# Optimization experiments

Measured on AMD Instinct MI355X. Metric: run time of the kernel, lower is better.

## Reference

```python
import jax, jax.numpy as jnp
import numpy as np

LATENT_N = 1024
COMMITMENT_COST = 1.0
TEMP = 0.1


def setup_inputs() -> dict:
    key = jax.random.key(0)
    k0, k1, k2, k3, k4, k5 = jax.random.split(key, 6)
    N, D, H, Fd, K = 65536, 1024, 128, 512, LATENT_N
    input_data = jax.random.normal(k0, (N, D), dtype=jnp.float32)
    W1 = jax.random.normal(k1, (D, H), dtype=jnp.float32) * (1.0 / np.sqrt(D))
    b1 = jnp.zeros((H,), dtype=jnp.float32)
    W2 = jax.random.normal(k2, (H, Fd), dtype=jnp.float32) * (1.0 / np.sqrt(H))
    b2 = jnp.zeros((Fd,), dtype=jnp.float32)
    code_book = jax.random.uniform(k3, (K, Fd), dtype=jnp.float32,
                                   minval=-1.0 / K, maxval=1.0 / K)
    return {"input_data": input_data, "W1": W1, "b1": b1,
            "W2": W2, "b2": b2, "code_book": code_book}


def reference(input_data, W1, b1, W2, b2, code_book):
    # feat MLP: Linear -> ReLU -> Linear
    z = jnp.matmul(jnp.maximum(jnp.matmul(input_data, W1) + b1, 0.0), W2) + b2  # [N, F]
    # squared L2 distances to codebook entries: [N, K]
    distances = (jnp.sum(z * z, axis=1, keepdims=True)
                 + jnp.sum(code_book * code_book, axis=1)
                 - 2.0 * jnp.matmul(z, code_book.T))
    logits = -distances / TEMP
    # categorical sample per row (softmax of logits)
    idx = jax.random.categorical(jax.random.key(42), logits, axis=-1)  # [N] int
    encodings = jax.nn.one_hot(idx, LATENT_N, dtype=z.dtype)  # [N, K]
    quantized = jnp.matmul(encodings, code_book)  # [N, F] == code_book[idx]
    e_latent_loss = jnp.mean((jax.lax.stop_gradient(quantized) - z) ** 2)
    q_latent_loss = jnp.mean((quantized - jax.lax.stop_gradient(z)) ** 2)
    loss = q_latent_loss + COMMITMENT_COST * e_latent_loss
    # straight-through estimator
    quantized_st = z + jax.lax.stop_gradient(quantized - z)
    avg_probs = jnp.mean(encodings, axis=0)  # [K]
    perplexity = jnp.exp(-jnp.sum(avg_probs * jnp.log(avg_probs + 1e-10)))
    return (loss, quantized_st, perplexity, encodings, -distances)
```

## Files before the change

kernel.cpp:

```cpp
#include <hip/hip_runtime.h>
#include <stdint.h>

#define N_ROWS 65536
#define DIM 1024
#define HID 128
#define FD 512
#define KCB 1024
#define HALFCNT 33554432u

#define OFF_Q    1
#define OFF_PERP 33554433
#define OFF_ENC  33554434
#define OFF_ND   100663298

typedef __attribute__((ext_vector_type(8))) short sh8;
typedef __attribute__((ext_vector_type(4))) float f32x4;

__device__ __forceinline__ uint32_t rotl32(uint32_t v, int r) { return (v << r) | (v >> (32 - r)); }

__device__ __forceinline__ void threefry(uint32_t c0, uint32_t c1, uint32_t& o0, uint32_t& o1) {
    const uint32_t ks0 = 0u, ks1 = 42u, ks2 = 0x1BD11BDAu ^ 0u ^ 42u;
    uint32_t x0 = c0 + ks0, x1 = c1 + ks1;
#define TFR(r) x0 += x1; x1 = rotl32(x1, r); x1 ^= x0;
    TFR(13) TFR(15) TFR(26) TFR(6)  x0 += ks1; x1 += ks2 + 1u;
    TFR(17) TFR(29) TFR(16) TFR(24) x0 += ks2; x1 += ks0 + 2u;
    TFR(13) TFR(15) TFR(26) TFR(6)  x0 += ks0; x1 += ks1 + 3u;
    TFR(17) TFR(29) TFR(16) TFR(24) x0 += ks1; x1 += ks2 + 4u;
    TFR(13) TFR(15) TFR(26) TFR(6)  x0 += ks2; x1 += ks0 + 5u;
#undef TFR
    o0 = x0; o1 = x1;
}

__device__ __forceinline__ float gumbel_f32(uint32_t b) {
    uint32_t m = b >> 9;
    float u = m ? (float)m * 1.1920928955078125e-07f : 1.17549435e-38f;
    const float LN2 = 0.6931471805599453f;
    return -LN2 * __log2f(-LN2 * __log2f(u));
}

__device__ __forceinline__ ushort bf16rne(float f) {
    uint32_t u = __float_as_uint(f);
    return (ushort)((u + 0x7FFFu + ((u >> 16) & 1u)) >> 16);
}
__device__ __forceinline__ uint32_t pack2rne(float a, float b) {
    return (uint32_t)bf16rne(a) | ((uint32_t)bf16rne(b) << 16);
}

__device__ __forceinline__ void async_cp16(const void* g, void* l) {
    __builtin_amdgcn_global_load_lds(
        (const __attribute__((address_space(1))) void*)g,
        (__attribute__((address_space(3))) void*)l, 16, 0, 0);
}

__global__ __launch_bounds__(256) void k_prep(const float* __restrict__ cb, const float* __restrict__ W1,
                                              const float* __restrict__ W2,
                                              ushort* __restrict__ cbh, double* __restrict__ cc,
                                              ushort* __restrict__ w1th, ushort* __restrict__ w2th,
                                              int* __restrict__ counts, double* __restrict__ lossb) {
    int gb = blockIdx.x, t = threadIdx.x;
    if (gb < 256) {
        int k = gb * 4 + (t >> 6), l = t & 63;
        const float4* row = (const float4*)(cb + (size_t)k * FD);
        float4 a = row[l * 2], b = row[l * 2 + 1];
        float v[8] = {a.x, a.y, a.z, a.w, b.x, b.y, b.z, b.w};
        double s = 0.0;
        uint32_t hu[4];
        #pragma unroll
        for (int e = 0; e < 4; ++e) {
            hu[e] = pack2rne(v[2 * e], v[2 * e + 1]);
            s = fma((double)v[2 * e], (double)v[2 * e], s);
            s = fma((double)v[2 * e + 1], (double)v[2 * e + 1], s);
        }
        *(uint4*)(cbh + (size_t)k * FD + l * 8) = make_uint4(hu[0], hu[1], hu[2], hu[3]);
        for (int off = 32; off; off >>= 1) s += __shfl_down(s, off, 64);
        if (l == 0) cc[k] = s;
    } else if (gb < 384) {
        int c = gb - 256;
        #pragma unroll
        for (int u = 0; u < 4; ++u) {
            int k = t + u * 256;
            w1th[(size_t)c * DIM + k] = bf16rne(W1[(size_t)k * HID + c]);
        }
    } else if (gb < 640) {
        int c = (gb - 384) * 2 + (t >> 7);
        int tt = t & 127;
        w2th[(size_t)c * HID + tt] = bf16rne(W2[(size_t)tt * FD + c]);
    } else {
        for (int k = t; k < KCB; k += 256) counts[k] = 0;
        lossb[t] = 0.0;
    }
}

__global__ __launch_bounds__(256) void kA(const float* __restrict__ X, const ushort* __restrict__ w1th,
                                          const float* __restrict__ b1, ushort* __restrict__ hh) {
    __shared__ __align__(16) char lds[32768];
    int t = threadIdx.x;
    int lane = t & 63, w = t >> 6;
    int wr = w >> 1, wc = w & 1;
    int n0 = blockIdx.x * 128;
    f32x4 zero4 = {0.f, 0.f, 0.f, 0.f};
    f32x4 acc[4][4];
    #pragma unroll
    for (int i = 0; i < 4; ++i)
        #pragma unroll
        for (int j = 0; j < 4; ++j) acc[i][j] = zero4;

    int xr = t >> 1;
    int cb0 = (t & 1) * 4;
    int xsw = xr & 7;

    for (int k0 = 0; k0 < DIM; k0 += 64) {
        #pragma unroll
        for (int i = 0; i < 4; ++i) {
            int rr = w * 32 + i * 8;
            int row = rr + (lane >> 3);
            int csrc = (lane & 7) ^ (row & 7);
            size_t goff = (size_t)row * DIM + k0 + csrc * 8;
            async_cp16(w1th + goff, lds + 16384 + rr * 128);
        }
        const float* xp = X + (size_t)(n0 + xr) * DIM + k0 + cb0 * 8;
        #pragma unroll
        for (int c = 0; c < 4; ++c) {
            float4 a = *(const float4*)(xp + c * 8);
            float4 b = *(const float4*)(xp + c * 8 + 4);
            uint4 hv;
            hv.x = pack2rne(a.x, a.y);
            hv.y = pack2rne(a.z, a.w);
            hv.z = pack2rne(b.x, b.y);
            hv.w = pack2rne(b.z, b.w);
            int slot = xr * 128 + (((cb0 + c) ^ xsw) << 4);
            *(uint4*)(lds + slot) = hv;
        }
        __syncthreads();
        #pragma unroll
        for (int kh = 0; kh < 2; ++kh) {
            int ch = kh * 4 + (lane >> 4);
            sh8 ah[4], bh[4];
            #pragma unroll
            for (int i = 0; i < 4; ++i) {
                int ra = wr * 64 + i * 16 + (lane & 15);
                ah[i] = *(const sh8*)(lds + ra * 128 + ((ch ^ (ra & 7)) << 4));
            }
            #pragma unroll
            for (int j = 0; j < 4; ++j) {
                int rb = wc * 64 + j * 16 + (lane & 15);
                bh[j] = *(const sh8*)(lds + 16384 + rb * 128 + ((ch ^ (rb & 7)) << 4));
            }
            #pragma unroll
            for (int i = 0; i < 4; ++i)
                #pragma unroll
                for (int j = 0; j < 4; ++j)
                    acc[i][j] = __builtin_amdgcn_mfma_f32_16x16x32_bf16(ah[i], bh[j], acc[i][j], 0, 0, 0);
        }
        __syncthreads();
    }
    int lane15 = lane & 15, lg = lane >> 4;
    #pragma unroll
    for (int j = 0; j < 4; ++j) {
        int gcol = wc * 64 + j * 16 + lane15;
        float b1v = b1[gcol];
        #pragma unroll
        for (int i = 0; i < 4; ++i)
            #pragma unroll
            for (int r = 0; r < 4; ++r) {
                int grow = n0 + wr * 64 + i * 16 + lg * 4 + r;
                hh[(size_t)grow * HID + gcol] = bf16rne(fmaxf(acc[i][j][r] + b1v, 0.f));
            }
    }
}

__global__ __launch_bounds__(256) void kB(const ushort* __restrict__ hh, const ushort* __restrict__ w2th,
                                          const float* __restrict__ b2,
                                          ushort* __restrict__ zbh, float* __restrict__ zz) {
    __shared__ __align__(16) char lds[8192];
    __shared__ float zzp[4][32];
    int t = threadIdx.x;
    int lane = t & 63, w = t >> 6;
    int n0 = blockIdx.x * 32;
    #pragma unroll
    for (int i = 0; i < 2; ++i) {
        int rr = w * 8 + i * 4;
        int row = rr + (lane >> 4);
        int csrc = (lane & 15) ^ (row & 7);
        size_t goff = (size_t)(n0 + row) * HID + csrc * 8;
        async_cp16(hh + goff, lds + rr * 256);
    }
    f32x4 zero4 = {0.f, 0.f, 0.f, 0.f};
    f32x4 acc[2][8];
    #pragma unroll
    for (int i = 0; i < 2; ++i)
        #pragma unroll
        for (int j = 0; j < 8; ++j) acc[i][j] = zero4;
    __syncthreads();
    #pragma unroll
    for (int kh = 0; kh < 4; ++kh) {
        int ch = kh * 4 + (lane >> 4);
        sh8 ah[2];
        #pragma unroll
        for (int i = 0; i < 2; ++i) {
            int ra = i * 16 + (lane & 15);
            ah[i] = *(const sh8*)(lds + ra * 256 + ((ch ^ (ra & 7)) << 4));
        }
        #pragma unroll
        for (int j = 0; j < 8; ++j) {
            int col = w * 128 + j * 16 + (lane & 15);
            sh8 bh = *(const sh8*)(w2th + (size_t)col * HID + ch * 8);
            #pragma unroll
            for (int i = 0; i < 2; ++i)
                acc[i][j] = __builtin_amdgcn_mfma_f32_16x16x32_bf16(ah[i], bh, acc[i][j], 0, 0, 0);
        }
    }
    int lane15 = lane & 15, lg = lane >> 4;
    float b2v[8];
    #pragma unroll
    for (int j = 0; j < 8; ++j) b2v[j] = b2[w * 128 + j * 16 + lane15];
    #pragma unroll
    for (int i = 0; i < 2; ++i)
        #pragma unroll
        for (int r = 0; r < 4; ++r) {
            int lrow = i * 16 + lg * 4 + r;
            size_t rowb = (size_t)(n0 + lrow) * FD;
            float s = 0.f;
            #pragma unroll
            for (int j = 0; j < 8; ++j) {
                float v = acc[i][j][r] + b2v[j];
                zbh[rowb + w * 128 + j * 16 + lane15] = bf16rne(v);
                s = fmaf(v, v, s);
            }
            s += __shfl_xor(s, 1, 64); s += __shfl_xor(s, 2, 64);
            s += __shfl_xor(s, 4, 64); s += __shfl_xor(s, 8, 64);
            if (lane15 == 0) zzp[w][lrow] = s;
        }
    __syncthreads();
    if (t < 32) zz[n0 + t] = zzp[0][t] + zzp[1][t] + zzp[2][t] + zzp[3][t];
}

__global__ __launch_bounds__(256) void k_mfma3(const ushort* __restrict__ zbh, const ushort* __restrict__ cbh,
                                               const float* __restrict__ zz, const double* __restrict__ cc,
                                               float* __restrict__ nd) {
    __shared__ __align__(16) char lds[32768];
    int t = threadIdx.x;
    int lane = t & 63, w = t >> 6;
    int wr = w >> 1, wc = w & 1;
    int bid = blockIdx.x;
    int bm = ((bid >> 6) << 3) | (bid & 7);
    int bkn = (bid >> 3) & 7;
    const ushort* Ahg = zbh + (size_t)bm * 128 * FD;
    const ushort* Bhg = cbh + (size_t)bkn * 128 * FD;

    f32x4 zero4 = {0.f, 0.f, 0.f, 0.f};
    f32x4 acc[4][4];
    #pragma unroll
    for (int i = 0; i < 4; ++i)
        #pragma unroll
        for (int j = 0; j < 4; ++j) acc[i][j] = zero4;

    for (int k0 = 0; k0 < FD; k0 += 64) {
        #pragma unroll
        for (int i = 0; i < 4; ++i) {
            int rr = w * 32 + i * 8;
            int row = rr + (lane >> 3);
            int csrc = (lane & 7) ^ (row & 7);
            size_t goff = (size_t)row * FD + k0 + csrc * 8;
            async_cp16(Ahg + goff, lds + rr * 128);
            async_cp16(Bhg + goff, lds + 16384 + rr * 128);
        }
        __syncthreads();
        #pragma unroll
        for (int kh = 0; kh < 2; ++kh) {
            int ch = kh * 4 + (lane >> 4);
            sh8 ah[4], bh[4];
            #pragma unroll
            for (int i = 0; i < 4; ++i) {
                int ra = wr * 64 + i * 16 + (lane & 15);
                ah[i] = *(const sh8*)(lds + ra * 128 + ((ch ^ (ra & 7)) << 4));
            }
            #pragma unroll
            for (int j = 0; j < 4; ++j) {
                int rb = wc * 64 + j * 16 + (lane & 15);
                bh[j] = *(const sh8*)(lds + 16384 + rb * 128 + ((ch ^ (rb & 7)) << 4));
            }
            #pragma unroll
            for (int i = 0; i < 4; ++i)
                #pragma unroll
                for (int j = 0; j < 4; ++j)
                    acc[i][j] = __builtin_amdgcn_mfma_f32_16x16x32_bf16(ah[i], bh[j], acc[i][j], 0, 0, 0);
        }
        __syncthreads();
    }
    int lane15 = lane & 15, lg = lane >> 4;
    int gcol[4];
    double ccv[4];
    #pragma unroll
    for (int j = 0; j < 4; ++j) {
        gcol[j] = bkn * 128 + wc * 64 + j * 16 + lane15;
        ccv[j] = cc[gcol[j]];
    }
    #pragma unroll
    for (int i = 0; i < 4; ++i)
        #pragma unroll
        for (int r = 0; r < 4; ++r) {
            int grow = bm * 128 + wr * 64 + i * 16 + lg * 4 + r;
            double zv = (double)zz[grow];
            size_t rowoff = (size_t)grow << 10;
            #pragma unroll
            for (int j = 0; j < 4; ++j)
                nd[rowoff + gcol[j]] = (float)(2.0 * (double)acc[i][j][r] - zv - ccv[j]);
        }
}

__global__ __launch_bounds__(256) void k_sample(const float* __restrict__ nd, const float* __restrict__ zz,
                                                int* __restrict__ idx, int* __restrict__ counts,
                                                double* __restrict__ lossb) {
    int n = blockIdx.x;
    int t = threadIdx.x;
    float zzn0 = zz[n], zzn1 = zz[n + 32768];
    float best0 = -1e30f, best1 = -1e30f;
    float bn0 = 0.f, bn1 = 0.f;
    int bi0 = 0, bi1 = 0;
    for (int k = t; k < KCB; k += 256) {
        uint32_t ctr = (uint32_t)(n * KCB + k);
        uint32_t r0, r1;
        threefry(ctr, ctr + HALFCNT, r0, r1);
        float g0 = gumbel_f32(r0), g1 = gumbel_f32(r1);
        float nd0 = nd[(size_t)n * KCB + k];
        float nd1 = nd[(size_t)(n + 32768) * KCB + k];
        float s0 = (nd0 + zzn0) * 10.0f + g0;
        float s1 = (nd1 + zzn1) * 10.0f + g1;
        if (s0 > best0) { best0 = s0; bi0 = k; bn0 = nd0; }
        if (s1 > best1) { best1 = s1; bi1 = k; bn1 = nd1; }
    }
    __shared__ float sv0[256], sv1[256], sn0[256], sn1[256];
    __shared__ int si0[256], si1[256];
    sv0[t] = best0; si0[t] = bi0; sn0[t] = bn0;
    sv1[t] = best1; si1[t] = bi1; sn1[t] = bn1;
    __syncthreads();
    for (int off = 128; off; off >>= 1) {
        if (t < off) {
            if (sv0[t + off] > sv0[t] || (sv0[t + off] == sv0[t] && si0[t + off] < si0[t])) {
                sv0[t] = sv0[t + off]; si0[t] = si0[t + off]; sn0[t] = sn0[t + off];
            }
            if (sv1[t + off] > sv1[t] || (sv1[t + off] == sv1[t] && si1[t + off] < si1[t])) {
                sv1[t] = sv1[t + off]; si1[t] = si1[t + off]; sn1[t] = sn1[t + off];
            }
        }
        __syncthreads();
    }
    if (t == 0) {
        idx[n] = si0[0];
        idx[n + 32768] = si1[0];
        atomicAdd(&counts[si0[0]], 1);
        atomicAdd(&counts[si1[0]], 1);
        atomicAdd(&lossb[n & 255], -(double)sn0[0] - (double)sn1[0]);
    }
}

__global__ __launch_bounds__(256) void k_enc(const int* __restrict__ idx, const float* __restrict__ cb,
                                             float* __restrict__ enc, float* __restrict__ qz) {
    int t = threadIdx.x;
    int n0 = blockIdx.x * 16;
    __shared__ int si[16];
    if (t < 16) si[t] = idx[n0 + t];
    __syncthreads();
    #pragma unroll
    for (int r = 0; r < 16; ++r) {
        int id = si[r];
        int base = t * 4;
        float4 v;
        v.x = (id == base)     ? 1.0f : 0.0f;
        v.y = (id == base + 1) ? 1.0f : 0.0f;
        v.z = (id == base + 2) ? 1.0f : 0.0f;
        v.w = (id == base + 3) ? 1.0f : 0.0f;
        *(float4*)&enc[(size_t)(n0 + r) * KCB + base] = v;
    }
    for (int e = t; e < 16 * 128; e += 256) {
        int r = e >> 7, s = e & 127;
        *(float4*)&qz[(size_t)(n0 + r) * FD + s * 4] =
            *(const float4*)&cb[(size_t)si[r] * FD + s * 4];
    }
}

__global__ void k_scalars(const int* __restrict__ counts, const double* __restrict__ lossb,
                          float* __restrict__ out) {
    int t = threadIdx.x;
    double s = 0.0;
    for (int k = t; k < KCB; k += 256) {
        double p = (double)counts[k] * (1.0 / 65536.0);
        s += p * log(p + 1e-10);
    }
    double lsum = lossb[t];
    for (int off = 32; off; off >>= 1) {
        s += __shfl_down(s, off, 64);
        lsum += __shfl_down(lsum, off, 64);
    }
    __shared__ double red[4], redl[4];
    int lane = t & 63, w = t >> 6;
    if (lane == 0) { red[w] = s; redl[w] = lsum; }
    __syncthreads();
    if (t == 0) {
        double tot = red[0] + red[1] + red[2] + red[3];
        double ltot = redl[0] + redl[1] + redl[2] + redl[3];
        out[OFF_PERP] = (float)exp(-tot);
        out[0] = (float)(ltot * (2.0 / 33554432.0));
    }
}

extern "C" void kernel_launch(void* const* d_in, const int* in_sizes, int n_in,
                              void* d_out, int out_size, void* d_ws, size_t ws_size,
                              hipStream_t stream) {
    const float* X  = (const float*)d_in[0];
    const float* W1 = (const float*)d_in[1];
    const float* b1 = (const float*)d_in[2];
    const float* W2 = (const float*)d_in[3];
    const float* b2 = (const float*)d_in[4];
    const float* cb = (const float*)d_in[5];

    float* out = (float*)d_out;
    float* qz  = out + (size_t)OFF_Q;
    float* enc = out + (size_t)OFF_ENC;
    float* nd  = out + (size_t)OFF_ND;

    float* zz = (float*)d_ws;
    double* cc = (double*)(zz + 65536);
    double* lossb = cc + 1024;
    int* counts = (int*)(lossb + 256);
    int* idx = counts + 1024;

    bool big_ws = ws_size >= ((size_t)100 << 20);
    ushort* ub = big_ws ? (ushort*)((char*)d_ws + (1 << 20)) : (ushort*)(enc + 2);
    ushort* zbh  = ub;
    ushort* cbh  = ub + 33554432;
    ushort* hh   = ub + 34078720;
    ushort* w1th = ub + 42467328;
    ushort* w2th = ub + 42598400;

    k_prep<<<641, 256, 0, stream>>>(cb, W1, W2, cbh, cc, w1th, w2th, counts, lossb);
    kA<<<512, 256, 0, stream>>>(X, w1th, b1, hh);
    kB<<<2048, 256, 0, stream>>>(hh, w2th, b2, zbh, zz);
    k_mfma3<<<4096, 256, 0, stream>>>(zbh, cbh, zz, cc, nd);
    k_sample<<<32768, 256, 0, stream>>>(nd, zz, idx, counts, lossb);
    k_enc<<<4096, 256, 0, stream>>>(idx, cb, enc, qz);
    k_scalars<<<1, 256, 0, stream>>>(counts, lossb, out);
}
```

Before: 472.8 us.

## Fuse MLP layers and fold Gumbel sampling into distance GEMM epilogue

Merges the two MLP kernels so the hidden activations stay in LDS instead of going through global memory. It also moves the Gumbel-max sampling into the distance GEMM epilogue, packing score and index into 64-bit keys and reducing them per row into a small partials buffer. A later kernel reduces those partials, updates counts and loss, and writes the encodings. This removes the separate sampling pass that re-read the 256MB distance matrix. In exchange the GEMM epilogue now does threefry hashing per element, and the second MLP layer reads W2 directly from global memory.

```diff
diff --git a/kernel.cpp b/kernel.cpp
--- a/kernel.cpp
+++ b/kernel.cpp
@@ -91,12 +91,16 @@
     }
 }
 
-__global__ __launch_bounds__(256) void kA(const float* __restrict__ X, const ushort* __restrict__ w1th,
-                                          const float* __restrict__ b1, ushort* __restrict__ hh) {
+__global__ __launch_bounds__(256) void kAB(const float* __restrict__ X, const ushort* __restrict__ w1th,
+                                           const float* __restrict__ b1, const ushort* __restrict__ w2th,
+                                           const float* __restrict__ b2,
+                                           ushort* __restrict__ zbh, float* __restrict__ zz) {
     __shared__ __align__(16) char lds[32768];
+    __shared__ float zzp[128][2];
     int t = threadIdx.x;
     int lane = t & 63, w = t >> 6;
     int wr = w >> 1, wc = w & 1;
+    int lane15 = lane & 15, lg = lane >> 4;
     int n0 = blockIdx.x * 128;
     f32x4 zero4 = {0.f, 0.f, 0.f, 0.f};
     f32x4 acc[4][4];
@@ -134,16 +138,16 @@
         __syncthreads();
         #pragma unroll
         for (int kh = 0; kh < 2; ++kh) {
-            int ch = kh * 4 + (lane >> 4);
+            int ch = kh * 4 + lg;
             sh8 ah[4], bh[4];
             #pragma unroll
             for (int i = 0; i < 4; ++i) {
-                int ra = wr * 64 + i * 16 + (lane & 15);
+                int ra = wr * 64 + i * 16 + lane15;
                 ah[i] = *(const sh8*)(lds + ra * 128 + ((ch ^ (ra & 7)) << 4));
             }
             #pragma unroll
             for (int j = 0; j < 4; ++j) {
-                int rb = wc * 64 + j * 16 + (lane & 15);
+                int rb = wc * 64 + j * 16 + lane15;
                 bh[j] = *(const sh8*)(lds + 16384 + rb * 128 + ((ch ^ (rb & 7)) << 4));
             }
             #pragma unroll
@@ -154,90 +158,80 @@
         }
         __syncthreads();
     }
-    int lane15 = lane & 15, lg = lane >> 4;
     #pragma unroll
     for (int j = 0; j < 4; ++j) {
-        int gcol = wc * 64 + j * 16 + lane15;
-        float b1v = b1[gcol];
+        int hcol = wc * 64 + j * 16 + lane15;
+        float b1v = b1[hcol];
+        int k8 = hcol >> 3, klo = hcol & 7;
         #pragma unroll
         for (int i = 0; i < 4; ++i)
             #pragma unroll
             for (int r = 0; r < 4; ++r) {
-                int grow = n0 + wr * 64 + i * 16 + lg * 4 + r;
-                hh[(size_t)grow * HID + gcol] = bf16rne(fmaxf(acc[i][j][r] + b1v, 0.f));
-            }
-    }
-}
-
-__global__ __launch_bounds__(256) void kB(const ushort* __restrict__ hh, const ushort* __restrict__ w2th,
-                                          const float* __restrict__ b2,
-                                          ushort* __restrict__ zbh, float* __restrict__ zz) {
-    __shared__ __align__(16) char lds[8192];
-    __shared__ float zzp[4][32];
-    int t = threadIdx.x;
-    int lane = t & 63, w = t >> 6;
-    int n0 = blockIdx.x * 32;
-    #pragma unroll
-    for (int i = 0; i < 2; ++i) {
-        int rr = w * 8 + i * 4;
-        int row = rr + (lane >> 4);
-        int csrc = (lane & 15) ^ (row & 7);
-        size_t goff = (size_t)(n0 + row) * HID + csrc * 8;
-        async_cp16(hh + goff, lds + rr * 256);
-    }
-    f32x4 zero4 = {0.f, 0.f, 0.f, 0.f};
-    f32x4 acc[2][8];
-    #pragma unroll
-    for (int i = 0; i < 2; ++i)
-        #pragma unroll
-        for (int j = 0; j < 8; ++j) acc[i][j] = zero4;
+                int row = wr * 64 + i * 16 + lg * 4 + r;
+                ushort hb = bf16rne(fmaxf(acc[i][j][r] + b1v, 0.f));
+                *(ushort*)(lds + row * 256 + ((k8 ^ (row & 7)) << 4) + klo * 2) = hb;
+            }
+    }
     __syncthreads();
-    #pragma unroll
-    for (int kh = 0; kh < 4; ++kh) {
-        int ch = kh * 4 + (lane >> 4);
-        sh8 ah[2];
-        #pragma unroll
-        for (int i = 0; i < 2; ++i) {
-            int ra = i * 16 + (lane & 15);
-            ah[i] = *(const sh8*)(lds + ra * 256 + ((ch ^ (ra & 7)) << 4));
-        }
-        #pragma unroll
-        for (int j = 0; j < 8; ++j) {
-            int col = w * 128 + j * 16 + (lane & 15);
-            sh8 bh = *(const sh8*)(w2th + (size_t)col * HID + ch * 8);
-            #pragma unroll
-            for (int i = 0; i < 2; ++i)
-                acc[i][j] = __builtin_amdgcn_mfma_f32_16x16x32_bf16(ah[i], bh, acc[i][j], 0, 0, 0);
-        }
-    }
-    int lane15 = lane & 15, lg = lane >> 4;
-    float b2v[8];
-    #pragma unroll
-    for (int j = 0; j < 8; ++j) b2v[j] = b2[w * 128 + j * 16 + lane15];
-    #pragma unroll
-    for (int i = 0; i < 2; ++i)
-        #pragma unroll
-        for (int r = 0; r < 4; ++r) {
-            int lrow = i * 16 + lg * 4 + r;
-            size_t rowb = (size_t)(n0 + lrow) * FD;
-            float s = 0.f;
-            #pragma unroll
-            for (int j = 0; j < 8; ++j) {
-                float v = acc[i][j][r] + b2v[j];
-                zbh[rowb + w * 128 + j * 16 + lane15] = bf16rne(v);
-                s = fmaf(v, v, s);
-            }
-            s += __shfl_xor(s, 1, 64); s += __shfl_xor(s, 2, 64);
-            s += __shfl_xor(s, 4, 64); s += __shfl_xor(s, 8, 64);
-            if (lane15 == 0) zzp[w][lrow] = s;
-        }
+    float zsum[16];
+    #pragma unroll
+    for (int e = 0; e < 16; ++e) zsum[e] = 0.f;
+    for (int c2 = 0; c2 < 4; ++c2) {
+        f32x4 acc2[4][4];
+        #pragma unroll
+        for (int i = 0; i < 4; ++i)
+            #pragma unroll
+            for (int j = 0; j < 4; ++j) acc2[i][j] = zero4;
+        #pragma unroll
+        for (int kh = 0; kh < 4; ++kh) {
+            int ch = kh * 4 + lg;
+            sh8 ah[4], bh[4];
+            #pragma unroll
+            for (int i = 0; i < 4; ++i) {
+                int ra = wr * 64 + i * 16 + lane15;
+                ah[i] = *(const sh8*)(lds + ra * 256 + ((ch ^ (ra & 7)) << 4));
+            }
+            #pragma unroll
+            for (int j = 0; j < 4; ++j) {
+                int col = c2 * 128 + wc * 64 + j * 16 + lane15;
+                bh[j] = *(const sh8*)(w2th + (size_t)col * HID + ch * 8);
+            }
+            #pragma unroll
+            for (int i = 0; i < 4; ++i)
+                #pragma unroll
+                for (int j = 0; j < 4; ++j)
+                    acc2[i][j] = __builtin_amdgcn_mfma_f32_16x16x32_bf16(ah[i], bh[j], acc2[i][j], 0, 0, 0);
+        }
+        #pragma unroll
+        for (int j = 0; j < 4; ++j) {
+            int col = c2 * 128 + wc * 64 + j * 16 + lane15;
+            float b2v = b2[col];
+            #pragma unroll
+            for (int i = 0; i < 4; ++i)
+                #pragma unroll
+                for (int r = 0; r < 4; ++r) {
+                    int row = wr * 64 + i * 16 + lg * 4 + r;
+                    float v = acc2[i][j][r] + b2v;
+                    zbh[(size_t)(n0 + row) * FD + col] = bf16rne(v);
+                    zsum[i * 4 + r] = fmaf(v, v, zsum[i * 4 + r]);
+                }
+        }
+    }
+    #pragma unroll
+    for (int e = 0; e < 16; ++e) {
+        float s = zsum[e];
+        s += __shfl_xor(s, 1, 64); s += __shfl_xor(s, 2, 64);
+        s += __shfl_xor(s, 4, 64); s += __shfl_xor(s, 8, 64);
+        if (lane15 == 0) zzp[wr * 64 + (e >> 2) * 16 + lg * 4 + (e & 3)][wc] = s;
+    }
     __syncthreads();
-    if (t < 32) zz[n0 + t] = zzp[0][t] + zzp[1][t] + zzp[2][t] + zzp[3][t];
-}
-
-__global__ __launch_bounds__(256) void k_mfma3(const ushort* __restrict__ zbh, const ushort* __restrict__ cbh,
-                                               const float* __restrict__ zz, const double* __restrict__ cc,
-                                               float* __restrict__ nd) {
+    if (t < 128) zz[n0 + t] = zzp[t][0] + zzp[t][1];
+}
+
+__global__ __launch_bounds__(256) void k_mfma3s(const ushort* __restrict__ zbh, const ushort* __restrict__ cbh,
+                                                const float* __restrict__ zz, const double* __restrict__ cc,
+                                                float* __restrict__ nd,
+                                                unsigned long long* __restrict__ partials) {
     __shared__ __align__(16) char lds[32768];
     int t = threadIdx.x;
     int lane = t & 63, w = t >> 6;
@@ -296,71 +290,63 @@
         gcol[j] = bkn * 128 + wc * 64 + j * 16 + lane15;
         ccv[j] = cc[gcol[j]];
     }
+    bool high = bm >= 256;
+    uint32_t csub = high ? HALFCNT : 0u;
     #pragma unroll
     for (int i = 0; i < 4; ++i)
         #pragma unroll
         for (int r = 0; r < 4; ++r) {
             int grow = bm * 128 + wr * 64 + i * 16 + lg * 4 + r;
-            double zv = (double)zz[grow];
+            float zzf = zz[grow];
+            double zv = (double)zzf;
             size_t rowoff = (size_t)grow << 10;
-            #pragma unroll
-            for (int j = 0; j < 4; ++j)
-                nd[rowoff + gcol[j]] = (float)(2.0 * (double)acc[i][j][r] - zv - ccv[j]);
-        }
-}
-
-__global__ __launch_bounds__(256) void k_sample(const float* __restrict__ nd, const float* __restrict__ zz,
-                                                int* __restrict__ idx, int* __restrict__ counts,
-                                                double* __restrict__ lossb) {
-    int n = blockIdx.x;
-    int t = threadIdx.x;
-    float zzn0 = zz[n], zzn1 = zz[n + 32768];
-    float best0 = -1e30f, best1 = -1e30f;
-    float bn0 = 0.f, bn1 = 0.f;
-    int bi0 = 0, bi1 = 0;
-    for (int k = t; k < KCB; k += 256) {
-        uint32_t ctr = (uint32_t)(n * KCB + k);
-        uint32_t r0, r1;
-        threefry(ctr, ctr + HALFCNT, r0, r1);
-        float g0 = gumbel_f32(r0), g1 = gumbel_f32(r1);
-        float nd0 = nd[(size_t)n * KCB + k];
-        float nd1 = nd[(size_t)(n + 32768) * KCB + k];
-        float s0 = (nd0 + zzn0) * 10.0f + g0;
-        float s1 = (nd1 + zzn1) * 10.0f + g1;
-        if (s0 > best0) { best0 = s0; bi0 = k; bn0 = nd0; }
-        if (s1 > best1) { best1 = s1; bi1 = k; bn1 = nd1; }
-    }
-    __shared__ float sv0[256], sv1[256], sn0[256], sn1[256];
-    __shared__ int si0[256], si1[256];
-    sv0[t] = best0; si0[t] = bi0; sn0[t] = bn0;
-    sv1[t] = best1; si1[t] = bi1; sn1[t] = bn1;
-    __syncthreads();
-    for (int off = 128; off; off >>= 1) {
-        if (t < off) {
-            if (sv0[t + off] > sv0[t] || (sv0[t + off] == sv0[t] && si0[t + off] < si0[t])) {
-                sv0[t] = sv0[t + off]; si0[t] = si0[t + off]; sn0[t] = sn0[t + off];
-            }
-            if (sv1[t + off] > sv1[t] || (sv1[t + off] == sv1[t] && si1[t + off] < si1[t])) {
-                sv1[t] = sv1[t + off]; si1[t] = si1[t + off]; sn1[t] = sn1[t + off];
-            }
-        }
-        __syncthreads();
-    }
-    if (t == 0) {
-        idx[n] = si0[0];
-        idx[n + 32768] = si1[0];
-        atomicAdd(&counts[si0[0]], 1);
-        atomicAdd(&counts[si1[0]], 1);
-        atomicAdd(&lossb[n & 255], -(double)sn0[0] - (double)sn1[0]);
-    }
-}
-
-__global__ __launch_bounds__(256) void k_enc(const int* __restrict__ idx, const float* __restrict__ cb,
-                                             float* __restrict__ enc, float* __restrict__ qz) {
+            unsigned long long bkey = 0ull;
+            #pragma unroll
+            for (int j = 0; j < 4; ++j) {
+                float ndf = (float)(2.0 * (double)acc[i][j][r] - zv - ccv[j]);
+                nd[rowoff + gcol[j]] = ndf;
+                uint32_t iflat = (uint32_t)grow * 1024u + (uint32_t)gcol[j];
+                uint32_t base = iflat - csub;
+                uint32_t r0, r1;
+                threefry(base, base + HALFCNT, r0, r1);
+                float gv = gumbel_f32(high ? r1 : r0);
+                float s = (ndf + zzf) * 10.0f + gv;
+                uint32_t ub = __float_as_uint(s);
+                ub ^= (uint32_t)(((int32_t)ub >> 31) | 0x80000000);
+                unsigned long long key = ((unsigned long long)ub << 32) | (uint32_t)(1023 - gcol[j]);
+                if (key > bkey) bkey = key;
+            }
+            #pragma unroll
+            for (int m = 1; m <= 8; m <<= 1) {
+                unsigned long long o = __shfl_xor(bkey, m, 64);
+                if (o > bkey) bkey = o;
+            }
+            if (lane15 == 0) partials[(size_t)grow * 16 + bkn * 2 + wc] = bkey;
+        }
+}
+
+__global__ __launch_bounds__(256) void k_enc2(const unsigned long long* __restrict__ partials,
+                                              const float* __restrict__ nd, const float* __restrict__ cb,
+                                              float* __restrict__ enc, float* __restrict__ qz,
+                                              int* __restrict__ counts, double* __restrict__ lossb) {
     int t = threadIdx.x;
     int n0 = blockIdx.x * 16;
     __shared__ int si[16];
-    if (t < 16) si[t] = idx[n0 + t];
+    if (t < 16) {
+        int n = n0 + t;
+        const unsigned long long* p = partials + (size_t)n * 16;
+        unsigned long long best = p[0];
+        #pragma unroll
+        for (int e = 1; e < 16; ++e) {
+            unsigned long long v = p[e];
+            if (v > best) best = v;
+        }
+        int k = 1023 - (int)(best & 0xFFFFFFFFull);
+        si[t] = k;
+        atomicAdd(&counts[k], 1);
+        float ndv = nd[(size_t)n * KCB + k];
+        atomicAdd(&lossb[n & 255], -(double)ndv);
+    }
     __syncthreads();
     #pragma unroll
     for (int r = 0; r < 16; ++r) {
@@ -424,21 +410,19 @@
     double* cc = (double*)(zz + 65536);
     double* lossb = cc + 1024;
     int* counts = (int*)(lossb + 256);
-    int* idx = counts + 1024;
 
     bool big_ws = ws_size >= ((size_t)100 << 20);
-    ushort* ub = big_ws ? (ushort*)((char*)d_ws + (1 << 20)) : (ushort*)(enc + 2);
+    char* big = big_ws ? ((char*)d_ws + (1 << 20)) : (char*)(enc + 2);
+    unsigned long long* partials = (unsigned long long*)big;
+    ushort* ub   = (ushort*)(big + ((size_t)9 << 20));
     ushort* zbh  = ub;
     ushort* cbh  = ub + 33554432;
-    ushort* hh   = ub + 34078720;
-    ushort* w1th = ub + 42467328;
-    ushort* w2th = ub + 42598400;
+    ushort* w1th = ub + 34078720;
+    ushort* w2th = ub + 34209792;
 
     k_prep<<<641, 256, 0, stream>>>(cb, W1, W2, cbh, cc, w1th, w2th, counts, lossb);
-    kA<<<512, 256, 0, stream>>>(X, w1th, b1, hh);
-    kB<<<2048, 256, 0, stream>>>(hh, w2th, b2, zbh, zz);
-    k_mfma3<<<4096, 256, 0, stream>>>(zbh, cbh, zz, cc, nd);
-    k_sample<<<32768, 256, 0, stream>>>(nd, zz, idx, counts, lossb);
-    k_enc<<<4096, 256, 0, stream>>>(idx, cb, enc, qz);
+    kAB<<<512, 256, 0, stream>>>(X, w1th, b1, w2th, b2, zbh, zz);
+    k_mfma3s<<<4096, 256, 0, stream>>>(zbh, cbh, zz, cc, nd, partials);
+    k_enc2<<<4096, 256, 0, stream>>>(partials, nd, cb, enc, qz, counts, lossb);
     k_scalars<<<1, 256, 0, stream>>>(counts, lossb, out);
 }
```

Result: no change. 472.1 us (-0.2%).
